# Kernel optimization log

Hardware: AMD Instinct MI355X
Metric: run time of the kernel (lower is better)

## Reference

```python
import jax, jax.numpy as jnp
import numpy as np

B, T, D = 4, 4096, 1024
H = 16
DH = D // H
F = 4096
EPS = 1e-5


def _layernorm(x, gamma, beta):
    mu = jnp.mean(x, axis=-1, keepdims=True)
    var = jnp.var(x, axis=-1, keepdims=True)
    return (x - mu) * jax.lax.rsqrt(var + EPS) * gamma + beta


def setup_inputs() -> dict:
    key = jax.random.key(0)
    ks = jax.random.split(key, 10)
    s = 0.02
    return {
        "x": jax.random.normal(ks[0], (B, T, D), dtype=jnp.float32),
        "Wqkv": jax.random.normal(ks[1], (D, 3 * D), dtype=jnp.float32) * s,
        "bqkv": jnp.zeros((3 * D,), dtype=jnp.float32),
        "Wo": jax.random.normal(ks[2], (D, D), dtype=jnp.float32) * s,
        "bo": jnp.zeros((D,), dtype=jnp.float32),
        "W1": jax.random.normal(ks[3], (D, F), dtype=jnp.float32) * s,
        "b1": jnp.zeros((F,), dtype=jnp.float32),
        "W2": jax.random.normal(ks[4], (F, D), dtype=jnp.float32) * s,
        "b2": jnp.zeros((D,), dtype=jnp.float32),
        "g1": jnp.ones((D,), dtype=jnp.float32),
        "be1": jnp.zeros((D,), dtype=jnp.float32),
        "g2": jnp.ones((D,), dtype=jnp.float32),
        "be2": jnp.zeros((D,), dtype=jnp.float32),
    }


def reference(x, Wqkv, bqkv, Wo, bo, W1, b1, W2, b2, g1, be1, g2, be2):
    # fused QKV projection: [B,T,3D]
    qkv = jnp.einsum("btd,de->bte", x, Wqkv) + bqkv
    q, k, v = jnp.split(qkv, 3, axis=-1)
    # [B,H,T,DH]
    q = q.reshape(B, T, H, DH).transpose(0, 2, 1, 3)
    k = k.reshape(B, T, H, DH).transpose(0, 2, 1, 3)
    v = v.reshape(B, T, H, DH).transpose(0, 2, 1, 3)
    scores = jnp.einsum("bhqd,bhkd->bhqk", q, k) / jnp.sqrt(jnp.float32(DH))
    attn = jax.nn.softmax(scores, axis=-1)
    ctx = jnp.einsum("bhqk,bhkd->bhqd", attn, v)
    ctx = ctx.transpose(0, 2, 1, 3).reshape(B, T, D)
    # output projection + residual + post-LN
    x = _layernorm(x + (jnp.einsum("btd,de->bte", ctx, Wo) + bo), g1, be1)
    # FFN (exact GELU, torch default) + residual + post-LN
    h = jax.nn.gelu(jnp.einsum("btd,df->btf", x, W1) + b1, approximate=False)
    ffn = jnp.einsum("btf,fd->btd", h, W2) + b2
    return _layernorm(x + ffn, g2, be2)
```

## Files before the change

### kernel.cpp

```cpp
#include <hip/hip_runtime.h>
#include <math.h>

typedef unsigned short u16;
typedef unsigned int   u32;
typedef __attribute__((ext_vector_type(8))) short short8;
typedef __attribute__((ext_vector_type(4))) float f32x4;

#define B_  4
#define T_  4096
#define D_  1024
#define H_  16
#define DH_ 64
#define F_  4096
#define EPS_ 1e-5f
#define QKV_LD (3 * D_)

#define QSCALE_ 0.18033688011112042f

__device__ __forceinline__ float b2f(u16 v) {
    union { u32 u; float f; } x; x.u = ((u32)v) << 16; return x.f;
}
__device__ __forceinline__ u16 f2b(float f) {
    union { u32 u; float f; } x; x.f = f;
    u32 r = (x.u >> 16) & 1u;
    return (u16)((x.u + 0x7fffu + r) >> 16);
}

__device__ __forceinline__ float ex2(float x) {
    float r;
    asm("v_exp_f32 %0, %1" : "=v"(r) : "v"(x));
    return r;
}
__device__ __forceinline__ float rcp_(float x) {
    float r;
    asm("v_rcp_f32 %0, %1" : "=v"(r) : "v"(x));
    return r;
}
__device__ __forceinline__ u32 cvtpk(float lo, float hi) {
    u32 r;
    asm("v_cvt_pk_bf16_f32 %0, %1, %2" : "=v"(r) : "v"(lo), "v"(hi));
    return r;
}
template<int CTRL>
__device__ __forceinline__ u32 dppu(u32 v) {
    return (u32)__builtin_amdgcn_update_dpp(0, (int)v, CTRL, 0xF, 0xF, true);
}

__device__ __forceinline__ float gelu_erf(float x) {
    const float z = fabsf(x) * 0.70710678118654752f;
    const float t = rcp_(1.0f + 0.3275911f * z);
    float poly = 1.061405429f;
    poly = poly * t - 1.453152027f;
    poly = poly * t + 1.421413741f;
    poly = poly * t - 0.284496736f;
    poly = poly * t + 0.254829592f;
    poly = poly * t;
    const float e = ex2(-z * z * 1.4426950408889634f);
    const float erfz = 1.0f - poly * e;
    const float se = copysignf(erfz, x);
    return 0.5f * x * (1.0f + se);
}

__device__ __forceinline__ void gll16(const u16* g, u16* ldsbase) {
    __builtin_amdgcn_global_load_lds(
        (const __attribute__((address_space(1))) void*)g,
        (__attribute__((address_space(3))) void*)ldsbase, 16, 0, 0);
}

__global__ __launch_bounds__(256) void conv_bf16_kernel(
    const float* __restrict__ in, u16* __restrict__ out)
{
    const int i = blockIdx.x * 256 + threadIdx.x;
    float4 v = ((const float4*)in)[i];
    ushort4 o;
    o.x = f2b(v.x); o.y = f2b(v.y); o.z = f2b(v.z); o.w = f2b(v.w);
    ((ushort4*)out)[i] = o;
}

__global__ __launch_bounds__(256) void transpose_bf16_kernel(
    const float* __restrict__ W, u16* __restrict__ Wt, int R, int C)
{
    __shared__ float tile[32][33];
    const int bx = blockIdx.x * 32;
    const int by = blockIdx.y * 32;
    const int tx = threadIdx.x & 31, ty = threadIdx.x >> 5;
#pragma unroll
    for (int p = 0; p < 4; ++p)
        tile[ty + p * 8][tx] = W[(size_t)(by + ty + p * 8) * C + bx + tx];
    __syncthreads();
#pragma unroll
    for (int p = 0; p < 4; ++p)
        Wt[(size_t)(bx + ty + p * 8) * R + by + tx] = f2b(tile[tx][ty + p * 8]);
}

template<bool CBF, int KU>
__global__ __launch_bounds__(256) void mfma_gemm(
    const u16* __restrict__ A, int lda,
    const u16* __restrict__ Bt, int ldbt,
    const float* __restrict__ bias,
    void* __restrict__ Cv, int ldc,
    int K, int act, int acc, int qcols)
{
    __shared__ __align__(16) u16 Al[KU][128 * 32];
    __shared__ __align__(16) u16 Bl[KU][128 * 32];

    const int tid  = threadIdx.x;
    const int lane = tid & 63, wave = tid >> 6;
    const int quad = lane >> 4, l16 = lane & 15;

    const int gx = gridDim.x;
    const int nwg = gx * gridDim.y;
    const int lin = blockIdx.y * gx + blockIdx.x;
    const int wg  = (lin & 7) * (nwg >> 3) + (lin >> 3);
    const int m0 = (wg / gx) * 128, n0 = (wg % gx) * 128;

    const int wm = (wave >> 1) * 64, wn = (wave & 1) * 64;

    int srow[2], sgk[2];
#pragma unroll
    for (int t = 0; t < 2; ++t) {
        const int c = wave * 128 + t * 64 + lane;
        srow[t] = c >> 2;
        sgk[t] = ((c & 3) ^ ((srow[t] >> 1) & 3)) * 8;
    }
    const u16* Ag = A  + (size_t)m0 * lda;
    const u16* Bg = Bt + (size_t)n0 * ldbt;
    const int apos = (quad ^ ((l16 >> 1) & 3)) * 8;

    f32x4 accr[4][4];
#pragma unroll
    for (int i = 0; i < 4; ++i)
#pragma unroll
        for (int j = 0; j < 4; ++j)
            accr[i][j] = (f32x4)(0.0f);

    for (int k0 = 0; k0 < K; k0 += 32 * KU) {
        __syncthreads();
#pragma unroll
        for (int h = 0; h < KU; ++h)
#pragma unroll
            for (int t = 0; t < 2; ++t) {
                gll16(Ag + (size_t)srow[t] * lda  + k0 + h * 32 + sgk[t],
                      &Al[h][(wave * 128 + t * 64) * 8]);
                gll16(Bg + (size_t)srow[t] * ldbt + k0 + h * 32 + sgk[t],
                      &Bl[h][(wave * 128 + t * 64) * 8]);
            }
        __syncthreads();

#pragma unroll
        for (int h = 0; h < KU; ++h) {
            short8 af[4], bf[4];
#pragma unroll
            for (int i = 0; i < 4; ++i)
                af[i] = *(const short8*)&Al[h][(wm + i * 16 + l16) * 32 + apos];
#pragma unroll
            for (int j = 0; j < 4; ++j)
                bf[j] = *(const short8*)&Bl[h][(wn + j * 16 + l16) * 32 + apos];
#pragma unroll
            for (int i = 0; i < 4; ++i)
#pragma unroll
                for (int j = 0; j < 4; ++j)
                    accr[i][j] = __builtin_amdgcn_mfma_f32_16x16x32_bf16(
                        af[i], bf[j], accr[i][j], 0, 0, 0);
        }
    }

#pragma unroll
    for (int j = 0; j < 4; ++j) {
        const int cc = n0 + wn + j * 16 + l16;
        float bv = acc ? 0.0f : bias[cc];
        const float sc = (cc < qcols) ? QSCALE_ : 1.0f;
#pragma unroll
        for (int i = 0; i < 4; ++i) {
#pragma unroll
            for (int r = 0; r < 4; ++r) {
                const int rr = m0 + wm + i * 16 + quad * 4 + r;
                float v = (accr[i][j][r] + bv) * sc;
                if (act == 1)
                    v = gelu_erf(v);
                if (CBF) {
                    ((u16*)Cv)[(size_t)rr * ldc + cc] = f2b(v);
                } else {
                    float* dst = (float*)Cv + (size_t)rr * ldc + cc;
                    if (acc) v += *dst;
                    *dst = v;
                }
            }
        }
    }
}

__global__ __launch_bounds__(512) void attn_mfma_kernel(
    const u16* __restrict__ qkv, u16* __restrict__ ctx)
{
    __shared__ u16 Ks[64 * 72];
    __shared__ u16 Vt[64 * 72];

    const int tid  = threadIdx.x;
    const int lane = tid & 63, wave = tid >> 6;
    const int quad = lane >> 4, l16 = lane & 15;
    const bool hi  = lane >= 32;
    const int bpa  = (lane ^ 32) << 2;

    const int gx = gridDim.x, gy = gridDim.y;
    const int nwg = gx * gy * gridDim.z;
    const int lin = (blockIdx.z * gy + blockIdx.y) * gx + blockIdx.x;
    const int wg  = (lin & 7) * (nwg >> 3) + (lin >> 3);
    const int q0 = (wg % gx) * 256;
    const int h  = (wg / gx) % gy;
    const int b  = wg / (gx * gy);

    short8 ones8;
#pragma unroll
    for (int i = 0; i < 8; ++i) ones8[i] = (short)0x3F80;

    short8 aq[2][2];
    {
        const u16* qb = qkv + (size_t)(b * T_ + q0 + wave * 32) * QKV_LD + h * DH_;
#pragma unroll
        for (int u = 0; u < 2; ++u)
#pragma unroll
            for (int s = 0; s < 2; ++s)
                aq[u][s] = *(const short8*)(qb + (size_t)(u * 16 + l16) * QKV_LD + s * 32 + quad * 8);
    }

    const int srow = tid >> 3;
    const int scol = (tid & 7) * 8;
    const int odd8 = srow & 1;
    const u16* kg = qkv + (size_t)(b * T_) * QKV_LD + D_     + h * DH_;
    const u16* vg = qkv + (size_t)(b * T_) * QKV_LD + 2 * D_ + h * DH_;

    short8 kreg, vreg;
    kreg = *(const short8*)(kg + (size_t)srow * QKV_LD + scol);
    vreg = *(const short8*)(vg + (size_t)srow * QKV_LD + scol);

    f32x4 o_acc[2][4];
#pragma unroll
    for (int u = 0; u < 2; ++u)
#pragma unroll
        for (int nt = 0; nt < 4; ++nt)
            o_acc[u][nt] = (f32x4)(0.0f);
    f32x4 l_acc[2];
    l_acc[0] = (f32x4)(0.0f);
    l_acc[1] = (f32x4)(0.0f);

    for (int kt = 0; kt < T_; kt += 64) {
        __syncthreads();
        {
            *(short8*)&Ks[srow * 72 + scol] = kreg;

            union { short8 s; u32 w[4]; } vv;
            vv.s = vreg;
            const u32 ws0 = dppu<0x118>(vv.w[0]);
            const u32 ws1 = dppu<0x118>(vv.w[1]);
            const u32 sl2 = dppu<0x108>(vv.w[2]);
            const u32 sl3 = dppu<0x108>(vv.w[3]);
            const int rowb = srow & ~1;
            const int sw = ((rowb & ~12) | ((rowb & 4) << 1) | ((rowb & 8) >> 1))
                           ^ ((rowb & 16) >> 2);
            const int koff = sw ^ scol;
#pragma unroll
            for (int J = 0; J < 4; ++J) {
                const u32 wj   = vv.w[J >> 1];
                const u32 wj4  = vv.w[2 + (J >> 1)];
                const u32 wsj  = (J >> 1) ? ws1 : ws0;
                const u32 slj4 = (J >> 1) ? sl3 : sl2;
                const u32 selfJ  = (J & 1) ? (wj   >> 16) : (wj   & 0xFFFFu);
                const u32 selfJ4 = (J & 1) ? (wj4  >> 16) : (wj4  & 0xFFFFu);
                const u32 nbrJ   = (J & 1) ? (wsj  >> 16) : (wsj  & 0xFFFFu);
                const u32 nbrJ4  = (J & 1) ? (slj4 >> 16) : (slj4 & 0xFFFFu);
                const u32 lo16 = odd8 ? nbrJ4  : selfJ;
                const u32 hi16 = odd8 ? selfJ4 : nbrJ;
                const int dh = scol + J + (odd8 ? 4 : 0);
                *(u32*)&Vt[dh * 72 + koff] = lo16 | (hi16 << 16);
            }
        }
        __syncthreads();

        if (kt + 64 < T_) {
            kreg = *(const short8*)(kg + (size_t)(kt + 64 + srow) * QKV_LD + scol);
            vreg = *(const short8*)(vg + (size_t)(kt + 64 + srow) * QKV_LD + scol);
        }

        f32x4 sa[2][4];
#pragma unroll
        for (int u = 0; u < 2; ++u)
#pragma unroll
            for (int nt = 0; nt < 4; ++nt)
                sa[u][nt] = (f32x4)(0.0f);
        __builtin_amdgcn_s_setprio(1);
#pragma unroll
        for (int s = 0; s < 2; ++s) {
            short8 kb[4];
#pragma unroll
            for (int nt = 0; nt < 4; ++nt)
                kb[nt] = *(const short8*)&Ks[(nt * 16 + l16) * 72 + s * 32 + quad * 8];
#pragma unroll
            for (int u = 0; u < 2; ++u)
#pragma unroll
                for (int nt = 0; nt < 4; ++nt)
                    sa[u][nt] = __builtin_amdgcn_mfma_f32_16x16x32_bf16(
                        kb[nt], aq[u][s], sa[u][nt], 0, 0, 0);
        }
        __builtin_amdgcn_s_setprio(0);

        u32 pk[2][4][2];
#pragma unroll
        for (int u = 0; u < 2; ++u)
#pragma unroll
            for (int nt = 0; nt < 4; ++nt)
#pragma unroll
                for (int w = 0; w < 2; ++w)
                    pk[u][nt][w] = cvtpk(ex2(sa[u][nt][2 * w]),
                                         ex2(sa[u][nt][2 * w + 1]));

        __builtin_amdgcn_s_setprio(1);
#pragma unroll
        for (int s = 0; s < 2; ++s) {
            short8 vb[4];
#pragma unroll
            for (int nt = 0; nt < 4; ++nt) {
                const int dh = nt * 16 + l16;
                vb[nt] = *(const short8*)&Vt[dh * 72 + ((s * 32 + quad * 8) ^ (dh & 56))];
            }
#pragma unroll
            for (int u = 0; u < 2; ++u) {
                union { u32 w[4]; short8 v; } pb;
                pb.w[0] = hi ? pk[u][2 * s + 1][0] : pk[u][2 * s][0];
                pb.w[1] = hi ? pk[u][2 * s + 1][1] : pk[u][2 * s][1];
                const u32 c0 = hi ? pk[u][2 * s][0] : pk[u][2 * s + 1][0];
                const u32 c1 = hi ? pk[u][2 * s][1] : pk[u][2 * s + 1][1];
                pb.w[2] = (u32)__builtin_amdgcn_ds_bpermute(bpa, (int)c0);
                pb.w[3] = (u32)__builtin_amdgcn_ds_bpermute(bpa, (int)c1);
                l_acc[u] = __builtin_amdgcn_mfma_f32_16x16x32_bf16(
                    ones8, pb.v, l_acc[u], 0, 0, 0);
#pragma unroll
                for (int nt = 0; nt < 4; ++nt)
                    o_acc[u][nt] = __builtin_amdgcn_mfma_f32_16x16x32_bf16(
                        vb[nt], pb.v, o_acc[u][nt], 0, 0, 0);
            }
        }
        __builtin_amdgcn_s_setprio(0);
    }

#pragma unroll
    for (int u = 0; u < 2; ++u) {
        const float inv = rcp_(l_acc[u][0]);
        const size_t qrow = (size_t)(b * T_ + q0 + wave * 32 + u * 16 + l16);
#pragma unroll
        for (int nt = 0; nt < 4; ++nt) {
            uint2 o;
            o.x = cvtpk(o_acc[u][nt][0] * inv, o_acc[u][nt][1] * inv);
            o.y = cvtpk(o_acc[u][nt][2] * inv, o_acc[u][nt][3] * inv);
            *(uint2*)&ctx[qrow * D_ + h * DH_ + nt * 16 + quad * 4] = o;
        }
    }
}

template<bool ABF, bool BBF, bool OBF>
__global__ __launch_bounds__(256) void add_ln_kernel(
    const void* __restrict__ av, const void* __restrict__ bv,
    const float* __restrict__ g, const float* __restrict__ be,
    void* __restrict__ outv)
{
    const int row = blockIdx.x;
    const int tid = threadIdx.x;

    float v[4];
    if (ABF) {
        ushort4 va = *(const ushort4*)((const u16*)av + (size_t)row * D_ + tid * 4);
        v[0] = b2f(va.x); v[1] = b2f(va.y); v[2] = b2f(va.z); v[3] = b2f(va.w);
    } else {
        float4 va = *(const float4*)((const float*)av + (size_t)row * D_ + tid * 4);
        v[0] = va.x; v[1] = va.y; v[2] = va.z; v[3] = va.w;
    }
    if (BBF) {
        ushort4 vb = *(const ushort4*)((const u16*)bv + (size_t)row * D_ + tid * 4);
        v[0] += b2f(vb.x); v[1] += b2f(vb.y); v[2] += b2f(vb.z); v[3] += b2f(vb.w);
    } else {
        float4 vb = *(const float4*)((const float*)bv + (size_t)row * D_ + tid * 4);
        v[0] += vb.x; v[1] += vb.y; v[2] += vb.z; v[3] += vb.w;
    }

    float s  = v[0] + v[1] + v[2] + v[3];
    float ss = v[0]*v[0] + v[1]*v[1] + v[2]*v[2] + v[3]*v[3];
#pragma unroll
    for (int off = 32; off > 0; off >>= 1) {
        s  += __shfl_down(s,  off, 64);
        ss += __shfl_down(ss, off, 64);
    }
    __shared__ float ws[4], wss[4], stats[2];
    const int wave = tid >> 6, lane = tid & 63;
    if (lane == 0) { ws[wave] = s; wss[wave] = ss; }
    __syncthreads();
    if (tid == 0) {
        float ts  = ws[0] + ws[1] + ws[2] + ws[3];
        float tss = wss[0] + wss[1] + wss[2] + wss[3];
        float mu  = ts * (1.0f / D_);
        float var = tss * (1.0f / D_) - mu * mu;
        stats[0] = mu;
        stats[1] = rsqrtf(var + EPS_);
    }
    __syncthreads();
    const float mu = stats[0], rs = stats[1];

    const float4 g4  = *(const float4*)(g  + tid * 4);
    const float4 be4 = *(const float4*)(be + tid * 4);
    float gg[4]  = {g4.x, g4.y, g4.z, g4.w};
    float beb[4] = {be4.x, be4.y, be4.z, be4.w};
    if (OBF) {
        ushort4 o;
        o.x = f2b((v[0] - mu) * rs * gg[0] + beb[0]);
        o.y = f2b((v[1] - mu) * rs * gg[1] + beb[1]);
        o.z = f2b((v[2] - mu) * rs * gg[2] + beb[2]);
        o.w = f2b((v[3] - mu) * rs * gg[3] + beb[3]);
        *(ushort4*)((u16*)outv + (size_t)row * D_ + tid * 4) = o;
    } else {
        float4 o;
        o.x = (v[0] - mu) * rs * gg[0] + beb[0];
        o.y = (v[1] - mu) * rs * gg[1] + beb[1];
        o.z = (v[2] - mu) * rs * gg[2] + beb[2];
        o.w = (v[3] - mu) * rs * gg[3] + beb[3];
        *(float4*)((float*)outv + (size_t)row * D_ + tid * 4) = o;
    }
}

extern "C" void kernel_launch(void* const* d_in, const int* in_sizes, int n_in,
                              void* d_out, int out_size, void* d_ws, size_t ws_size,
                              hipStream_t stream)
{
    const float* x    = (const float*)d_in[0];
    const float* Wqkv = (const float*)d_in[1];
    const float* bqkv = (const float*)d_in[2];
    const float* Wo   = (const float*)d_in[3];
    const float* bo   = (const float*)d_in[4];
    const float* W1   = (const float*)d_in[5];
    const float* b1   = (const float*)d_in[6];
    const float* W2   = (const float*)d_in[7];
    const float* b2   = (const float*)d_in[8];
    const float* g1   = (const float*)d_in[9];
    const float* be1  = (const float*)d_in[10];
    const float* g2   = (const float*)d_in[11];
    const float* be2  = (const float*)d_in[12];
    float* out = (float*)d_out;

    const int M = B_ * T_;
    char* ws = (char*)d_ws;
    char* sc = (char*)d_out;

    u16*   qkvB   = (u16*)ws;
    u16*   ctxB   = (u16*)(ws + (size_t)100663296);
    float* proj   = (float*)ws;
    u16*   x1B    = (u16*)(ws + (size_t)100663296);
    u16*   hchunk = (u16*)ws;
    u16*   ffnB   = (u16*)(ws + (size_t)67108864);

    u16* xB    = (u16*)sc;
    u16* WqkvT = (u16*)(sc + (size_t)33554432);
    u16* WoT   = (u16*)(sc + (size_t)39845888);
    u16* W1T   = (u16*)(sc + (size_t)41943040);
    u16* W2T   = (u16*)(sc + (size_t)50331648);

    dim3 blk(256);

    conv_bf16_kernel<<<dim3(M * D_ / 1024), blk, 0, stream>>>(x, xB);
    transpose_bf16_kernel<<<dim3(3 * D_ / 32, D_ / 32), blk, 0, stream>>>(Wqkv, WqkvT, D_, 3 * D_);
    transpose_bf16_kernel<<<dim3(D_ / 32, D_ / 32), blk, 0, stream>>>(Wo, WoT, D_, D_);
    transpose_bf16_kernel<<<dim3(F_ / 32, D_ / 32), blk, 0, stream>>>(W1, W1T, D_, F_);
    transpose_bf16_kernel<<<dim3(D_ / 32, F_ / 32), blk, 0, stream>>>(W2, W2T, F_, D_);

    mfma_gemm<true, 1><<<dim3(3 * D_ / 128, M / 128), blk, 0, stream>>>(
        xB, D_, WqkvT, D_, bqkv, qkvB, 3 * D_, D_, 0, 0, D_);

    attn_mfma_kernel<<<dim3(T_ / 256, H_, B_), dim3(512), 0, stream>>>(qkvB, ctxB);

    mfma_gemm<false, 1><<<dim3(D_ / 128, M / 128), blk, 0, stream>>>(
        ctxB, D_, WoT, D_, bo, proj, D_, D_, 0, 0, 0);

    add_ln_kernel<false, false, true><<<dim3(M), blk, 0, stream>>>(x, proj, g1, be1, x1B);

    for (int mc = 0; mc < 2; ++mc) {
        const size_t m0 = (size_t)mc * 8192;
        mfma_gemm<true, 1><<<dim3(F_ / 128, 8192 / 128), blk, 0, stream>>>(
            x1B + m0 * D_, D_, W1T, D_, b1, hchunk, F_, D_, 1, 0, 0);
        mfma_gemm<true, 2><<<dim3(D_ / 128, 8192 / 128), blk, 0, stream>>>(
            hchunk, F_, W2T, F_, b2, ffnB + m0 * D_, D_, F_, 0, 0, 0);
    }

    add_ln_kernel<true, true, false><<<dim3(M), blk, 0, stream>>>(x1B, ffnB, g2, be2, out);
}
```

Baseline: 1.014 ms.

## Add 256x256-tile double-buffered MFMA GEMM for QKV, Wo and W1 projections

Introduces a new GEMM kernel with 256x256 output tiles and 512 threads. It double-buffers A and B tiles in LDS through direct global-to-LDS loads, uses XOR-swizzled layouts and a grouped workgroup remap, and interleaves the next-tile prefetch with MFMA phases under raised wave priority. The larger tiles are meant to improve operand reuse and raise MFMA utilisation for the QKV, output-projection and W1 GEMMs. The W2 GEMM keeps the old kernel. The cost is heavy LDS use (128KB per block), which limits occupancy, plus many barriers per K-step.

```diff
diff --git a/kernel.cpp b/kernel.cpp
--- a/kernel.cpp
+++ b/kernel.cpp
@@ -184,6 +184,127 @@
                     float* dst = (float*)Cv + (size_t)rr * ldc + cc;
                     if (acc) v += *dst;
                     *dst = v;
+                }
+            }
+        }
+    }
+}
+
+template<bool CBF>
+__global__ __launch_bounds__(512, 2) void mfma_gemm256(
+    const u16* __restrict__ A, int lda,
+    const u16* __restrict__ Bt, int ldbt,
+    const float* __restrict__ bias,
+    void* __restrict__ Cv, int ldc,
+    int K, int act, int qcols)
+{
+    __shared__ __align__(16) u16 Al[2][256 * 64];
+    __shared__ __align__(16) u16 Bl[2][256 * 64];
+
+    const int tid  = threadIdx.x;
+    const int lane = tid & 63, wave = tid >> 6;
+    const int quad = lane >> 4, l16 = lane & 15;
+
+    const int gx = gridDim.x;
+    const int nwg = gx * gridDim.y;
+    const int lin = blockIdx.y * gx + blockIdx.x;
+    const int wg  = (lin & 7) * (nwg >> 3) + (lin >> 3);
+    const int m0 = (wg / gx) * 256, n0 = (wg % gx) * 256;
+
+    const int wm = (wave >> 2) * 128;
+    const int wn = (wave & 3) * 64;
+
+    const int sr   = lane >> 3;
+    const int soct = ((lane & 7) ^ (sr & 7)) * 8;
+    const int lrow0 = wave * 16;
+
+#define STAGE_HALF(Gp, ld, baseRow, k0_, Ldst) do {                            \
+        _Pragma("unroll")                                                      \
+        for (int c = 0; c < 2; ++c) {                                          \
+            gll16((Gp) + (size_t)((baseRow) + lrow0 + c * 8 + sr) * (ld)       \
+                       + (k0_) + soct,                                         \
+                  (Ldst) + (lrow0 + c * 8) * 64);                              \
+        }                                                                      \
+    } while (0)
+
+    f32x4 accr[8][4];
+#pragma unroll
+    for (int i = 0; i < 8; ++i)
+#pragma unroll
+        for (int j = 0; j < 4; ++j)
+            accr[i][j] = (f32x4)(0.0f);
+
+    const int nt = K >> 6;
+
+    STAGE_HALF(A,  lda,  m0,       0, &Al[0][0]);
+    STAGE_HALF(A,  lda,  m0 + 128, 0, &Al[0][128 * 64]);
+    STAGE_HALF(Bt, ldbt, n0,       0, &Bl[0][0]);
+    STAGE_HALF(Bt, ldbt, n0 + 128, 0, &Bl[0][128 * 64]);
+
+    for (int t = 0; t < nt; ++t) {
+        const int cur = t & 1, nxt = cur ^ 1;
+        const int k1 = (t + 1) * 64;
+        const bool more = (t + 1 < nt);
+
+        short8 bf[4];
+#pragma unroll
+        for (int p = 0; p < 4; ++p) {
+            if (more) {
+                if      (p == 0) STAGE_HALF(A,  lda,  m0,       k1, &Al[nxt][0]);
+                else if (p == 1) STAGE_HALF(A,  lda,  m0 + 128, k1, &Al[nxt][128 * 64]);
+                else if (p == 2) STAGE_HALF(Bt, ldbt, n0,       k1, &Bl[nxt][0]);
+                else             STAGE_HALF(Bt, ldbt, n0 + 128, k1, &Bl[nxt][128 * 64]);
+            }
+            if (p == 0) {
+                if (more) asm volatile("s_waitcnt vmcnt(2)" ::: "memory");
+                else      asm volatile("s_waitcnt vmcnt(0)" ::: "memory");
+            }
+            asm volatile("s_barrier" ::: "memory");
+
+            const int mh = p & 1, ks = p >> 1;
+            const int roct = (((ks << 2) | quad) ^ (l16 & 7)) * 8;
+            const u16* ab = &Al[cur][(wm + mh * 64) * 64];
+            short8 af[4];
+#pragma unroll
+            for (int i = 0; i < 4; ++i)
+                af[i] = *(const short8*)&ab[(i * 16 + l16) * 64 + roct];
+            if (mh == 0) {
+                const u16* bb = &Bl[cur][wn * 64];
+#pragma unroll
+                for (int j = 0; j < 4; ++j)
+                    bf[j] = *(const short8*)&bb[(j * 16 + l16) * 64 + roct];
+            }
+
+            __builtin_amdgcn_s_setprio(1);
+#pragma unroll
+            for (int i = 0; i < 4; ++i)
+#pragma unroll
+                for (int j = 0; j < 4; ++j)
+                    accr[mh * 4 + i][j] = __builtin_amdgcn_mfma_f32_16x16x32_bf16(
+                        af[i], bf[j], accr[mh * 4 + i][j], 0, 0, 0);
+            __builtin_amdgcn_s_setprio(0);
+            asm volatile("s_barrier" ::: "memory");
+        }
+    }
+#undef STAGE_HALF
+
+#pragma unroll
+    for (int j = 0; j < 4; ++j) {
+        const int cc = n0 + wn + j * 16 + l16;
+        const float bv = bias[cc];
+        const float sc = (cc < qcols) ? QSCALE_ : 1.0f;
+#pragma unroll
+        for (int idx = 0; idx < 8; ++idx) {
+            const int rbase = m0 + wm + (idx >> 2) * 64 + (idx & 3) * 16 + quad * 4;
+#pragma unroll
+            for (int r = 0; r < 4; ++r) {
+                float v = (accr[idx][j][r] + bv) * sc;
+                if (act == 1)
+                    v = gelu_erf(v);
+                if (CBF) {
+                    ((u16*)Cv)[(size_t)(rbase + r) * ldc + cc] = f2b(v);
+                } else {
+                    ((float*)Cv)[(size_t)(rbase + r) * ldc + cc] = v;
                 }
             }
         }
@@ -462,6 +583,7 @@
     u16* W2T   = (u16*)(sc + (size_t)50331648);
 
     dim3 blk(256);
+    dim3 gblk(512);
 
     conv_bf16_kernel<<<dim3(M * D_ / 1024), blk, 0, stream>>>(x, xB);
     transpose_bf16_kernel<<<dim3(3 * D_ / 32, D_ / 32), blk, 0, stream>>>(Wqkv, WqkvT, D_, 3 * D_);
@@ -469,20 +591,20 @@
     transpose_bf16_kernel<<<dim3(F_ / 32, D_ / 32), blk, 0, stream>>>(W1, W1T, D_, F_);
     transpose_bf16_kernel<<<dim3(D_ / 32, F_ / 32), blk, 0, stream>>>(W2, W2T, F_, D_);
 
-    mfma_gemm<true, 1><<<dim3(3 * D_ / 128, M / 128), blk, 0, stream>>>(
-        xB, D_, WqkvT, D_, bqkv, qkvB, 3 * D_, D_, 0, 0, D_);
-
-    attn_mfma_kernel<<<dim3(T_ / 256, H_, B_), dim3(512), 0, stream>>>(qkvB, ctxB);
-
-    mfma_gemm<false, 1><<<dim3(D_ / 128, M / 128), blk, 0, stream>>>(
-        ctxB, D_, WoT, D_, bo, proj, D_, D_, 0, 0, 0);
+    mfma_gemm256<true><<<dim3(3 * D_ / 256, M / 256), gblk, 0, stream>>>(
+        xB, D_, WqkvT, D_, bqkv, qkvB, 3 * D_, D_, 0, D_);
+
+    attn_mfma_kernel<<<dim3(T_ / 256, H_, B_), gblk, 0, stream>>>(qkvB, ctxB);
+
+    mfma_gemm256<false><<<dim3(D_ / 256, M / 256), gblk, 0, stream>>>(
+        ctxB, D_, WoT, D_, bo, proj, D_, D_, 0, 0);
 
     add_ln_kernel<false, false, true><<<dim3(M), blk, 0, stream>>>(x, proj, g1, be1, x1B);
 
     for (int mc = 0; mc < 2; ++mc) {
         const size_t m0 = (size_t)mc * 8192;
-        mfma_gemm<true, 1><<<dim3(F_ / 128, 8192 / 128), blk, 0, stream>>>(
-            x1B + m0 * D_, D_, W1T, D_, b1, hchunk, F_, D_, 1, 0, 0);
+        mfma_gemm256<true><<<dim3(F_ / 256, 8192 / 256), gblk, 0, stream>>>(
+            x1B + m0 * D_, D_, W1T, D_, b1, hchunk, F_, D_, 1, 0);
         mfma_gemm<true, 2><<<dim3(D_ / 128, 8192 / 128), blk, 0, stream>>>(
             hchunk, F_, W2T, F_, b2, ffnB + m0 * D_, D_, F_, 0, 0, 0);
     }
```

Result: no change. 1.013 ms (-0.1%).

## Widen attention key tile to 128 and emit Wo projection in bf16

Applied to the files above, without the earlier changes.

The attention kernel now stages 128 keys per iteration in shared memory (two 64-row halves), so it needs half as many barrier pairs and global prefetch rounds per key sweep. The inner QK/softmax/PV compute runs twice per staged tile. Separately, the output-projection GEMM writes bf16 instead of fp32, and the first add+LayerNorm reads bf16, which halves that intermediate's memory traffic. The costs are more shared memory and registers per block, and some loss of precision in the projection output before the residual add.

```diff
diff --git a/kernel.cpp b/kernel.cpp
--- a/kernel.cpp
+++ b/kernel.cpp
@@ -193,8 +193,8 @@
 __global__ __launch_bounds__(512) void attn_mfma_kernel(
     const u16* __restrict__ qkv, u16* __restrict__ ctx)
 {
-    __shared__ u16 Ks[64 * 72];
-    __shared__ u16 Vt[64 * 72];
+    __shared__ u16 Ks[128 * 72];
+    __shared__ u16 Vt[64 * 144];
 
     const int tid  = threadIdx.x;
     const int lane = tid & 63, wave = tid >> 6;
@@ -230,9 +230,12 @@
     const u16* kg = qkv + (size_t)(b * T_) * QKV_LD + D_     + h * DH_;
     const u16* vg = qkv + (size_t)(b * T_) * QKV_LD + 2 * D_ + h * DH_;
 
-    short8 kreg, vreg;
-    kreg = *(const short8*)(kg + (size_t)srow * QKV_LD + scol);
-    vreg = *(const short8*)(vg + (size_t)srow * QKV_LD + scol);
+    short8 kreg[2], vreg[2];
+#pragma unroll
+    for (int hh = 0; hh < 2; ++hh) {
+        kreg[hh] = *(const short8*)(kg + (size_t)(hh * 64 + srow) * QKV_LD + scol);
+        vreg[hh] = *(const short8*)(vg + (size_t)(hh * 64 + srow) * QKV_LD + scol);
+    }
 
     f32x4 o_acc[2][4];
 #pragma unroll
@@ -244,18 +247,20 @@
     l_acc[0] = (f32x4)(0.0f);
     l_acc[1] = (f32x4)(0.0f);
 
-    for (int kt = 0; kt < T_; kt += 64) {
+    for (int kt = 0; kt < T_; kt += 128) {
         __syncthreads();
-        {
-            *(short8*)&Ks[srow * 72 + scol] = kreg;
+#pragma unroll
+        for (int hh = 0; hh < 2; ++hh) {
+            const int row = hh * 64 + srow;
+            *(short8*)&Ks[row * 72 + scol] = kreg[hh];
 
             union { short8 s; u32 w[4]; } vv;
-            vv.s = vreg;
+            vv.s = vreg[hh];
             const u32 ws0 = dppu<0x118>(vv.w[0]);
             const u32 ws1 = dppu<0x118>(vv.w[1]);
             const u32 sl2 = dppu<0x108>(vv.w[2]);
             const u32 sl3 = dppu<0x108>(vv.w[3]);
-            const int rowb = srow & ~1;
+            const int rowb = row & ~1;
             const int sw = ((rowb & ~12) | ((rowb & 4) << 1) | ((rowb & 8) >> 1))
                            ^ ((rowb & 16) >> 2);
             const int koff = sw ^ scol;
@@ -272,75 +277,82 @@
                 const u32 lo16 = odd8 ? nbrJ4  : selfJ;
                 const u32 hi16 = odd8 ? selfJ4 : nbrJ;
                 const int dh = scol + J + (odd8 ? 4 : 0);
-                *(u32*)&Vt[dh * 72 + koff] = lo16 | (hi16 << 16);
+                *(u32*)&Vt[dh * 144 + koff] = lo16 | (hi16 << 16);
             }
         }
         __syncthreads();
 
-        if (kt + 64 < T_) {
-            kreg = *(const short8*)(kg + (size_t)(kt + 64 + srow) * QKV_LD + scol);
-            vreg = *(const short8*)(vg + (size_t)(kt + 64 + srow) * QKV_LD + scol);
-        }
-
-        f32x4 sa[2][4];
-#pragma unroll
-        for (int u = 0; u < 2; ++u)
-#pragma unroll
-            for (int nt = 0; nt < 4; ++nt)
-                sa[u][nt] = (f32x4)(0.0f);
-        __builtin_amdgcn_s_setprio(1);
-#pragma unroll
-        for (int s = 0; s < 2; ++s) {
-            short8 kb[4];
-#pragma unroll
-            for (int nt = 0; nt < 4; ++nt)
-                kb[nt] = *(const short8*)&Ks[(nt * 16 + l16) * 72 + s * 32 + quad * 8];
-#pragma unroll
-            for (int u = 0; u < 2; ++u)
-#pragma unroll
-                for (int nt = 0; nt < 4; ++nt)
-                    sa[u][nt] = __builtin_amdgcn_mfma_f32_16x16x32_bf16(
-                        kb[nt], aq[u][s], sa[u][nt], 0, 0, 0);
-        }
-        __builtin_amdgcn_s_setprio(0);
-
-        u32 pk[2][4][2];
-#pragma unroll
-        for (int u = 0; u < 2; ++u)
-#pragma unroll
-            for (int nt = 0; nt < 4; ++nt)
-#pragma unroll
-                for (int w = 0; w < 2; ++w)
-                    pk[u][nt][w] = cvtpk(ex2(sa[u][nt][2 * w]),
-                                         ex2(sa[u][nt][2 * w + 1]));
-
-        __builtin_amdgcn_s_setprio(1);
-#pragma unroll
-        for (int s = 0; s < 2; ++s) {
-            short8 vb[4];
-#pragma unroll
-            for (int nt = 0; nt < 4; ++nt) {
-                const int dh = nt * 16 + l16;
-                vb[nt] = *(const short8*)&Vt[dh * 72 + ((s * 32 + quad * 8) ^ (dh & 56))];
-            }
-#pragma unroll
-            for (int u = 0; u < 2; ++u) {
-                union { u32 w[4]; short8 v; } pb;
-                pb.w[0] = hi ? pk[u][2 * s + 1][0] : pk[u][2 * s][0];
-                pb.w[1] = hi ? pk[u][2 * s + 1][1] : pk[u][2 * s][1];
-                const u32 c0 = hi ? pk[u][2 * s][0] : pk[u][2 * s + 1][0];
-                const u32 c1 = hi ? pk[u][2 * s][1] : pk[u][2 * s + 1][1];
-                pb.w[2] = (u32)__builtin_amdgcn_ds_bpermute(bpa, (int)c0);
-                pb.w[3] = (u32)__builtin_amdgcn_ds_bpermute(bpa, (int)c1);
-                l_acc[u] = __builtin_amdgcn_mfma_f32_16x16x32_bf16(
-                    ones8, pb.v, l_acc[u], 0, 0, 0);
-#pragma unroll
-                for (int nt = 0; nt < 4; ++nt)
-                    o_acc[u][nt] = __builtin_amdgcn_mfma_f32_16x16x32_bf16(
-                        vb[nt], pb.v, o_acc[u][nt], 0, 0, 0);
+        if (kt + 128 < T_) {
+#pragma unroll
+            for (int hh = 0; hh < 2; ++hh) {
+                kreg[hh] = *(const short8*)(kg + (size_t)(kt + 128 + hh * 64 + srow) * QKV_LD + scol);
+                vreg[hh] = *(const short8*)(vg + (size_t)(kt + 128 + hh * 64 + srow) * QKV_LD + scol);
             }
         }
-        __builtin_amdgcn_s_setprio(0);
+
+#pragma unroll
+        for (int s2 = 0; s2 < 2; ++s2) {
+            f32x4 sa[2][4];
+#pragma unroll
+            for (int u = 0; u < 2; ++u)
+#pragma unroll
+                for (int nt = 0; nt < 4; ++nt)
+                    sa[u][nt] = (f32x4)(0.0f);
+            __builtin_amdgcn_s_setprio(1);
+#pragma unroll
+            for (int s = 0; s < 2; ++s) {
+                short8 kb[4];
+#pragma unroll
+                for (int nt = 0; nt < 4; ++nt)
+                    kb[nt] = *(const short8*)&Ks[(s2 * 64 + nt * 16 + l16) * 72 + s * 32 + quad * 8];
+#pragma unroll
+                for (int u = 0; u < 2; ++u)
+#pragma unroll
+                    for (int nt = 0; nt < 4; ++nt)
+                        sa[u][nt] = __builtin_amdgcn_mfma_f32_16x16x32_bf16(
+                            kb[nt], aq[u][s], sa[u][nt], 0, 0, 0);
+            }
+            __builtin_amdgcn_s_setprio(0);
+
+            u32 pk[2][4][2];
+#pragma unroll
+            for (int u = 0; u < 2; ++u)
+#pragma unroll
+                for (int nt = 0; nt < 4; ++nt)
+#pragma unroll
+                    for (int w = 0; w < 2; ++w)
+                        pk[u][nt][w] = cvtpk(ex2(sa[u][nt][2 * w]),
+                                             ex2(sa[u][nt][2 * w + 1]));
+
+            __builtin_amdgcn_s_setprio(1);
+#pragma unroll
+            for (int s = 0; s < 2; ++s) {
+                short8 vb[4];
+#pragma unroll
+                for (int nt = 0; nt < 4; ++nt) {
+                    const int dh = nt * 16 + l16;
+                    vb[nt] = *(const short8*)&Vt[dh * 144 + s2 * 64
+                                                 + (((s * 32 + quad * 8)) ^ (dh & 56))];
+                }
+#pragma unroll
+                for (int u = 0; u < 2; ++u) {
+                    union { u32 w[4]; short8 v; } pb;
+                    pb.w[0] = hi ? pk[u][2 * s + 1][0] : pk[u][2 * s][0];
+                    pb.w[1] = hi ? pk[u][2 * s + 1][1] : pk[u][2 * s][1];
+                    const u32 c0 = hi ? pk[u][2 * s][0] : pk[u][2 * s + 1][0];
+                    const u32 c1 = hi ? pk[u][2 * s][1] : pk[u][2 * s + 1][1];
+                    pb.w[2] = (u32)__builtin_amdgcn_ds_bpermute(bpa, (int)c0);
+                    pb.w[3] = (u32)__builtin_amdgcn_ds_bpermute(bpa, (int)c1);
+                    l_acc[u] = __builtin_amdgcn_mfma_f32_16x16x32_bf16(
+                        ones8, pb.v, l_acc[u], 0, 0, 0);
+#pragma unroll
+                    for (int nt = 0; nt < 4; ++nt)
+                        o_acc[u][nt] = __builtin_amdgcn_mfma_f32_16x16x32_bf16(
+                            vb[nt], pb.v, o_acc[u][nt], 0, 0, 0);
+                }
+            }
+            __builtin_amdgcn_s_setprio(0);
+        }
     }
 
 #pragma unroll
@@ -450,7 +462,7 @@
 
     u16*   qkvB   = (u16*)ws;
     u16*   ctxB   = (u16*)(ws + (size_t)100663296);
-    float* proj   = (float*)ws;
+    u16*   projB  = (u16*)ws;
     u16*   x1B    = (u16*)(ws + (size_t)100663296);
     u16*   hchunk = (u16*)ws;
     u16*   ffnB   = (u16*)(ws + (size_t)67108864);
@@ -474,10 +486,10 @@
 
     attn_mfma_kernel<<<dim3(T_ / 256, H_, B_), dim3(512), 0, stream>>>(qkvB, ctxB);
 
-    mfma_gemm<false, 1><<<dim3(D_ / 128, M / 128), blk, 0, stream>>>(
-        ctxB, D_, WoT, D_, bo, proj, D_, D_, 0, 0, 0);
-
-    add_ln_kernel<false, false, true><<<dim3(M), blk, 0, stream>>>(x, proj, g1, be1, x1B);
+    mfma_gemm<true, 1><<<dim3(D_ / 128, M / 128), blk, 0, stream>>>(
+        ctxB, D_, WoT, D_, bo, projB, D_, D_, 0, 0, 0);
+
+    add_ln_kernel<false, true, true><<<dim3(M), blk, 0, stream>>>(x, projB, g1, be1, x1B);
 
     for (int mc = 0; mc < 2; ++mc) {
         const size_t m0 = (size_t)mc * 8192;
```

Measured after the change: 1.008 ms. About the same (-0.6%).
